# Optimization experiments

Measured on AMD Instinct MI355X. Metric: run time of the kernel, lower is better.

## Reference

```python
import jax, jax.numpy as jnp
import numpy as np

ALPHA = 0.2  # LeakyReLU negative slope
NEG_INF = -1e12


def setup_inputs() -> dict:
    key = jax.random.key(0)
    k1, k2, k3, k4 = jax.random.split(key, 4)
    B, N, F_in, F_out = 8, 4096, 128, 64
    inp = jax.random.normal(k1, (B, N, F_in), dtype=jnp.float32)
    adj = jax.random.randint(k2, (B, N, N), 0, 2, dtype=jnp.int32)
    # xavier-uniform-ish init for W, a
    W = jax.random.normal(k3, (F_in, F_out), dtype=jnp.float32) * (2.0 / (F_in + F_out)) ** 0.5
    a = jax.random.normal(k4, (2 * F_out, 1), dtype=jnp.float32) * (2.0 / (2 * F_out + 1)) ** 0.5
    return {"inp": inp, "adj": adj, "W": W, "a": a}


def reference(inp, adj, W, a):
    # inp: [B,N,F_in], adj: [B,N,N] int, W: [F_in,F_out], a: [2*F_out,1]
    F_out = W.shape[1]
    h = jnp.einsum('bnf,fo->bno', inp, W)          # [B,N,F_out]
    a1 = a[:F_out, 0]                              # [F_out]
    a2 = a[F_out:, 0]                              # [F_out]
    # e[b,i,j] = leakyrelu(h_i . a1 + h_j . a2)  (== concat([h_i,h_j]) @ a)
    s1 = h @ a1                                    # [B,N]
    s2 = h @ a2                                    # [B,N]
    e = s1[:, :, None] + s2[:, None, :]            # [B,N,N]
    e = jnp.where(e > 0, e, ALPHA * e)             # LeakyReLU
    att = jnp.where(adj > 0, e, NEG_INF)
    att = jax.nn.softmax(att, axis=-1)             # [B,N,N]
    # dropout p=0.0 -> identity
    h_prime = jnp.einsum('bij,bjo->bio', att, h)   # [B,N,F_out]
    return jax.nn.elu(h_prime)
```

## Files before the change

### kernel.cpp

```cpp
#include <hip/hip_runtime.h>
#include <hip/hip_bf16.h>
#include <hip/hip_fp16.h>
#include <cstdint>

typedef __attribute__((ext_vector_type(8))) short short8;
typedef __attribute__((ext_vector_type(4))) float floatx4;
typedef __attribute__((ext_vector_type(4))) int   intx4;

#define LEAKY_ALPHA 0.2f

__device__ __forceinline__ unsigned short f2bf_rne(float f) {
    unsigned u = __float_as_uint(f);
    unsigned r = u + 0x7FFFu + ((u >> 16) & 1u);
    return (unsigned short)(r >> 16);
}

__device__ __forceinline__ unsigned pk2bf(float lo, float hi) {
    union { __hip_bfloat162 b; unsigned u; } c;
    c.b = __float22bfloat162_rn(make_float2(lo, hi));
    return c.u;
}

__device__ __forceinline__ float2 h2f2(unsigned w) {
    union { unsigned u; __half2 h; } c; c.u = w;
    return __half22float2(c.h);
}


__global__ __launch_bounds__(256) void k_h(const float* __restrict__ inp,
                                           const float* __restrict__ W,
                                           const float* __restrict__ a,
                                           unsigned short* __restrict__ hT,
                                           float2* __restrict__ e1,
                                           __half2* __restrict__ e2h) {
    __shared__ float hs[64][65];
    const int tid  = threadIdx.x;
    const int wv   = tid >> 6;
    const int lane = tid & 63;
    const int blk  = blockIdx.x;
    const int b     = blk >> 6;
    const int ibase = (blk & 63) * 64;

    const float a1 = a[lane];
    const float a2 = a[64 + lane];

    for (int rr = 0; rr < 16; ++rr) {
        const int rloc = wv * 16 + rr;
        const int row  = ibase + rloc;
        const float* ip = inp + ((size_t)(b * 4096 + row)) * 128;
        float acc = 0.f;
        #pragma unroll
        for (int f = 0; f < 128; f += 4) {
            float4 v = *(const float4*)(ip + f);
            acc += v.x * W[(f + 0) * 64 + lane];
            acc += v.y * W[(f + 1) * 64 + lane];
            acc += v.z * W[(f + 2) * 64 + lane];
            acc += v.w * W[(f + 3) * 64 + lane];
        }
        hs[rloc][lane] = acc;
        float r1 = acc * a1;
        float r2 = acc * a2;
        #pragma unroll
        for (int off = 32; off > 0; off >>= 1) {
            r1 += __shfl_xor(r1, off);
            r2 += __shfl_xor(r2, off);
        }
        if (lane == 0) {
            e1[b * 4096 + row]  = make_float2(__expf(r1), __expf(LEAKY_ALPHA * r1));
            e2h[b * 4096 + row] = __floats2half2_rn(__expf(r2), __expf(LEAKY_ALPHA * r2));
        }
    }
    __syncthreads();

    const int o    = tid & 63;
    const int half = tid >> 6;
    const int tl   = half >> 1;
    const int nco  = (half & 1) * 16;
    unsigned pk[8];
    #pragma unroll
    for (int s = 0; s < 16; s += 2) {
        const int n0 = nco + s, n1 = nco + s + 1;
        const int c0 = 4 * (n0 & 7) + (n0 >> 3);
        const int c1 = 4 * (n1 & 7) + (n1 >> 3);
        unsigned lo = f2bf_rne(hs[tl * 32 + c0][o]);
        unsigned hi = f2bf_rne(hs[tl * 32 + c1][o]);
        pk[s >> 1] = lo | (hi << 16);
    }
    const int tile = (ibase >> 5) + tl;
    unsigned short* dst = hT + (((size_t)b * 128 + tile) * 64 + o) * 32 + nco;
    *(int4*)(dst)     = *(int4*)&pk[0];
    *(int4*)(dst + 8) = *(int4*)&pk[4];
}

__global__ __launch_bounds__(256, 4) void k_fused(const int* __restrict__ adj,
                                                  const unsigned short* __restrict__ hT,
                                                  const float2* __restrict__ e1g,
                                                  const __half2* __restrict__ e2hg,
                                                  float* __restrict__ out) {
    __shared__ unsigned long long mask64[32][16][4];
    __shared__ unsigned e2su[4096];

    const int tid   = threadIdx.x;
    const int b     = blockIdx.x >> 7;
    const int rtile = blockIdx.x & 127;
    const int wv    = tid >> 6;
    const int lane  = tid & 63;

    {
        const unsigned* src = (const unsigned*)(e2hg + b * 4096);
        #pragma unroll
        for (int t = 0; t < 4; ++t) {
            const int c0 = tid * 16 + t * 4;
            const int4 raw = *(const int4*)(src + c0);
            const int base = (c0 & ~31) + ((c0 & 31) >> 2);
            e2su[base +  0] = (unsigned)raw.x;
            e2su[base +  8] = (unsigned)raw.y;
            e2su[base + 16] = (unsigned)raw.z;
            e2su[base + 24] = (unsigned)raw.w;
        }
    }

    {
        const int* abase = adj + ((size_t)(b * 4096 + rtile * 32)) * 4096;
        for (int r = 0; r < 8; ++r) {
            const int lr = wv * 8 + r;
            const int* prow = abase + (size_t)lr * 4096 + lane * 4;
            #pragma unroll 4
            for (int g = 0; g < 16; ++g) {
                const intx4 v = __builtin_nontemporal_load((const intx4*)(prow + g * 256));
                const unsigned long long b0 = __ballot(v.x > 0);
                const unsigned long long b1 = __ballot(v.y > 0);
                const unsigned long long b2 = __ballot(v.z > 0);
                const unsigned long long b3 = __ballot(v.w > 0);
                if (lane == 0) {
                    ulonglong2* d = (ulonglong2*)&mask64[lr][g][0];
                    ulonglong2 t0; t0.x = b0; t0.y = b1;
                    ulonglong2 t1; t1.x = b2; t1.y = b3;
                    d[0] = t0; d[1] = t1;
                }
            }
        }
    }

    const int jhalf = wv >> 1;
    const int m     = lane & 15;
    const int kh    = lane >> 4;
    const int rl    = (wv & 1) * 16 + m;
    const int rbase = rtile * 32 + (wv & 1) * 16;
    const int row   = rbase + m;

    const float2 E1 = e1g[b * 4096 + row];
    const float E1p = E1.x, E1n = E1.y;
    const int jb0 = jhalf * 2048 + kh * 8;

    const unsigned short* hbase =
        hT + (((size_t)b * 128 + jhalf * 64) * 64 + m) * 32 + kh * 8;
    const unsigned short* hrow0 = hbase;
    const unsigned short* hrow1 = hbase + 512;
    const unsigned short* hrow2 = hbase + 1024;
    const unsigned short* hrow3 = hbase + 1536;

    floatx4 acc0 = (floatx4){0.f,0.f,0.f,0.f};
    floatx4 acc1 = (floatx4){0.f,0.f,0.f,0.f};
    floatx4 acc2 = (floatx4){0.f,0.f,0.f,0.f};
    floatx4 acc3 = (floatx4){0.f,0.f,0.f,0.f};
    float lsum = 0.f;

    short8 rb0_0, rb1_0, rb2_0, rb3_0, rb0_1, rb1_1, rb2_1, rb3_1;
    rb0_0 = *(const short8*)(hrow0);         rb1_0 = *(const short8*)(hrow1);
    rb2_0 = *(const short8*)(hrow2);         rb3_0 = *(const short8*)(hrow3);
    rb0_1 = *(const short8*)(hrow0 + 2048);  rb1_1 = *(const short8*)(hrow1 + 2048);
    rb2_1 = *(const short8*)(hrow2 + 2048);  rb3_1 = *(const short8*)(hrow3 + 2048);

    __syncthreads();

#define GAT_COL(WRD, T)                                                        \
    {                                                                          \
        const float2 ef = h2f2((unsigned)(WRD));                               \
        const float P  = E1p * ef.x;                                           \
        const float Nn = E1n * ef.y;                                           \
        float p = (P > 1.0f) ? P : Nn;                                         \
        p = ((mb >> (T)) & 1u) ? p : 0.0f;                                     \
        psum += p;                                                             \
        pv[T] = p;                                                             \
    }

#define GAT_STEP(SL, STEPIDX)                                                  \
    do {                                                                       \
        const short8 cb0 = rb0_##SL, cb1 = rb1_##SL;                           \
        const short8 cb2 = rb2_##SL, cb3 = rb3_##SL;                           \
        const int pstep = ((STEPIDX) + 2) & 63;         \
        const int poff = pstep * 2048;                         \
        rb0_##SL = *(const short8*)(hrow0 + poff);                             \
        rb1_##SL = *(const short8*)(hrow1 + poff);                             \
        rb2_##SL = *(const short8*)(hrow2 + poff);                             \
        rb3_##SL = *(const short8*)(hrow3 + poff);                             \
        const int soff = jb0 + (STEPIDX) * 32;                                 \
        const int4 eA = *(const int4*)&e2su[soff];                             \
        const int4 eB = *(const int4*)&e2su[soff + 4];                         \
        const unsigned mb = (unsigned)(Mcur >> (8 * ((STEPIDX) & 7))) & 0xffu; \
        float pv[8];                                                           \
        float psum = 0.f;                                                      \
        GAT_COL(eA.x, 0) GAT_COL(eA.y, 1) GAT_COL(eA.z, 2) GAT_COL(eA.w, 3)    \
        GAT_COL(eB.x, 4) GAT_COL(eB.y, 5) GAT_COL(eB.z, 6) GAT_COL(eB.w, 7)    \
        lsum += psum;                                                          \
        int4 ai;                                                               \
        ai.x = pk2bf(pv[0], pv[1]); ai.y = pk2bf(pv[2], pv[3]);                \
        ai.z = pk2bf(pv[4], pv[5]); ai.w = pk2bf(pv[6], pv[7]);                \
        union { int4 i; short8 s; } cc; cc.i = ai;                             \
        const short8 af = cc.s;                                                \
        acc0 = __builtin_amdgcn_mfma_f32_16x16x32_bf16(af, cb0, acc0, 0,0,0);  \
        acc1 = __builtin_amdgcn_mfma_f32_16x16x32_bf16(af, cb1, acc1, 0,0,0);  \
        acc2 = __builtin_amdgcn_mfma_f32_16x16x32_bf16(af, cb2, acc2, 0,0,0);  \
        acc3 = __builtin_amdgcn_mfma_f32_16x16x32_bf16(af, cb3, acc3, 0,0,0);  \
    } while (0)

    #pragma unroll 1
    for (int p = 0; p < 8; ++p) {
        const unsigned long long Mcur =
            *(const unsigned long long*)&mask64[rl][jhalf * 8 + p][kh];
        #pragma unroll
        for (int q = 0; q < 4; ++q) {
            GAT_STEP(0, p * 8 + 2 * q);
            GAT_STEP(1, p * 8 + 2 * q + 1);
        }
    }
#undef GAT_STEP
#undef GAT_COL

    lsum += __shfl_xor(lsum, 16);
    lsum += __shfl_xor(lsum, 32);

    floatx4 accs[4] = {acc0, acc1, acc2, acc3};

    float* accb = (float*)&mask64[0][0][0];
    float* lb   = accb + 2 * 64 * 17;

    __syncthreads();
    if (wv >= 2) {
        #pragma unroll
        for (int f = 0; f < 4; ++f)
            #pragma unroll
            for (int r = 0; r < 4; ++r)
                accb[(wv - 2) * 64 * 17 + lane * 17 + f * 4 + r] = accs[f][r];
        lb[(wv - 2) * 64 + lane] = lsum;
    }
    __syncthreads();
    if (wv < 2) {
        const float ltot = lsum + lb[wv * 64 + lane];
        #pragma unroll
        for (int f = 0; f < 4; ++f) {
            #pragma unroll
            for (int r = 0; r < 4; ++r) {
                float v = accs[f][r] + accb[wv * 64 * 17 + lane * 17 + f * 4 + r];
                const int drow = (lane >> 4) * 4 + r;
                const float lr = __shfl(ltot, drow);
                const float hp = v / lr;
                const float o  = (hp > 0.f) ? hp : (__expf(hp) - 1.f);
                out[((size_t)(b * 4096 + rbase + drow)) * 64 + f * 16 + (lane & 15)] = o;
            }
        }
    }
}

extern "C" void kernel_launch(void* const* d_in, const int* in_sizes, int n_in,
                              void* d_out, int out_size, void* d_ws, size_t ws_size,
                              hipStream_t stream) {
    const float* inp = (const float*)d_in[0];
    const int*   adj = (const int*)d_in[1];
    const float* W   = (const float*)d_in[2];
    const float* a   = (const float*)d_in[3];
    float* out = (float*)d_out;

    unsigned short* hT = (unsigned short*)d_ws;
    float2*  e1  = (float2*)((char*)d_ws + (size_t)4 * 1024 * 1024);
    __half2* e2h = (__half2*)((char*)d_ws + (size_t)4 * 1024 * 1024 + 262144);

    k_h<<<512, 256, 0, stream>>>(inp, W, a, hT, e1, e2h);
    k_fused<<<1024, 256, 0, stream>>>(adj, hT, e1, e2h, out);
}
```

Before: 790.7 us.

## Overlap adjacency mask packing with attention MFMA loop via software pipelining

Moves the adjacency-to-bitmask packing out of the prologue and interleaves it with the main gather/MFMA loop. Each iteration prefetches the next 256-column group of adj rows while computing on the current group. Wave pairs now split columns by interleaved 32-column parity instead of contiguous halves, so each mask group is consumed right after it is built. This aims to hide the large adj HBM read latency behind compute, at the cost of more live registers (eight intx4 loads in flight) and a __syncthreads per group.

After: 830.0 us. 5.0% more time.

```diff
diff --git a/kernel.cpp b/kernel.cpp
--- a/kernel.cpp
+++ b/kernel.cpp
@@ -106,6 +106,62 @@
     const int wv    = tid >> 6;
     const int lane  = tid & 63;
 
+    const int par  = wv >> 1;
+    const int m    = lane & 15;
+    const int kh   = lane >> 4;
+    const int khs  = kh << 3;
+    const int sh8  = par << 3;
+    const int rl   = (wv & 1) * 16 + m;
+    const int rbase = rtile * 32 + (wv & 1) * 16;
+    const int row   = rbase + m;
+
+    const int* pA = adj + ((size_t)(b * 4096 + rtile * 32 + wv * 8)) * 4096 + lane * 4;
+
+    intx4 av0, av1, av2, av3, av4, av5, av6, av7;
+
+#define PACK_ISSUE_LO(GOFF)                                                    \
+    do {                                                                       \
+        const int* pg = pA + (GOFF);                                           \
+        av0 = __builtin_nontemporal_load((const intx4*)(pg + 0 * 4096));       \
+        av1 = __builtin_nontemporal_load((const intx4*)(pg + 1 * 4096));       \
+        av2 = __builtin_nontemporal_load((const intx4*)(pg + 2 * 4096));       \
+        av3 = __builtin_nontemporal_load((const intx4*)(pg + 3 * 4096));       \
+    } while (0)
+
+#define PACK_ISSUE_HI(GOFF)                                                    \
+    do {                                                                       \
+        const int* pg = pA + (GOFF);                                           \
+        av4 = __builtin_nontemporal_load((const intx4*)(pg + 4 * 4096));       \
+        av5 = __builtin_nontemporal_load((const intx4*)(pg + 5 * 4096));       \
+        av6 = __builtin_nontemporal_load((const intx4*)(pg + 6 * 4096));       \
+        av7 = __builtin_nontemporal_load((const intx4*)(pg + 7 * 4096));       \
+    } while (0)
+
+#define PB_ROW(R, G, AV)                                                       \
+    {                                                                          \
+        const unsigned long long b0 = __ballot(AV.x > 0);                      \
+        const unsigned long long b1 = __ballot(AV.y > 0);                      \
+        const unsigned long long b2 = __ballot(AV.z > 0);                      \
+        const unsigned long long b3 = __ballot(AV.w > 0);                      \
+        if (lane == 0) {                                                       \
+            ulonglong2* d = (ulonglong2*)&mask64[wv * 8 + (R)][(G)][0];        \
+            ulonglong2 t0; t0.x = b0; t0.y = b1;                               \
+            ulonglong2 t1; t1.x = b2; t1.y = b3;                               \
+            d[0] = t0; d[1] = t1;                                              \
+        }                                                                      \
+    }
+
+#define PACK_BALLOT_LO(G)                                                      \
+    do { PB_ROW(0, G, av0) PB_ROW(1, G, av1)                                   \
+         PB_ROW(2, G, av2) PB_ROW(3, G, av3) } while (0)
+
+#define PACK_BALLOT_HI(G)                                                      \
+    do { PB_ROW(4, G, av4) PB_ROW(5, G, av5)                                   \
+         PB_ROW(6, G, av6) PB_ROW(7, G, av7) } while (0)
+
+    PACK_ISSUE_LO(0);
+    PACK_ISSUE_HI(0);
+
     {
         const unsigned* src = (const unsigned*)(e2hg + b * 4096);
         #pragma unroll
@@ -120,41 +176,11 @@
         }
     }
 
-    {
-        const int* abase = adj + ((size_t)(b * 4096 + rtile * 32)) * 4096;
-        for (int r = 0; r < 8; ++r) {
-            const int lr = wv * 8 + r;
-            const int* prow = abase + (size_t)lr * 4096 + lane * 4;
-            #pragma unroll 4
-            for (int g = 0; g < 16; ++g) {
-                const intx4 v = __builtin_nontemporal_load((const intx4*)(prow + g * 256));
-                const unsigned long long b0 = __ballot(v.x > 0);
-                const unsigned long long b1 = __ballot(v.y > 0);
-                const unsigned long long b2 = __ballot(v.z > 0);
-                const unsigned long long b3 = __ballot(v.w > 0);
-                if (lane == 0) {
-                    ulonglong2* d = (ulonglong2*)&mask64[lr][g][0];
-                    ulonglong2 t0; t0.x = b0; t0.y = b1;
-                    ulonglong2 t1; t1.x = b2; t1.y = b3;
-                    d[0] = t0; d[1] = t1;
-                }
-            }
-        }
-    }
-
-    const int jhalf = wv >> 1;
-    const int m     = lane & 15;
-    const int kh    = lane >> 4;
-    const int rl    = (wv & 1) * 16 + m;
-    const int rbase = rtile * 32 + (wv & 1) * 16;
-    const int row   = rbase + m;
-
     const float2 E1 = e1g[b * 4096 + row];
     const float E1p = E1.x, E1n = E1.y;
-    const int jb0 = jhalf * 2048 + kh * 8;
 
     const unsigned short* hbase =
-        hT + (((size_t)b * 128 + jhalf * 64) * 64 + m) * 32 + kh * 8;
+        hT + (((size_t)b * 128) * 64 + m) * 32 + khs;
     const unsigned short* hrow0 = hbase;
     const unsigned short* hrow1 = hbase + 512;
     const unsigned short* hrow2 = hbase + 1024;
@@ -167,11 +193,16 @@
     float lsum = 0.f;
 
     short8 rb0_0, rb1_0, rb2_0, rb3_0, rb0_1, rb1_1, rb2_1, rb3_1;
-    rb0_0 = *(const short8*)(hrow0);         rb1_0 = *(const short8*)(hrow1);
-    rb2_0 = *(const short8*)(hrow2);         rb3_0 = *(const short8*)(hrow3);
-    rb0_1 = *(const short8*)(hrow0 + 2048);  rb1_1 = *(const short8*)(hrow1 + 2048);
-    rb2_1 = *(const short8*)(hrow2 + 2048);  rb3_1 = *(const short8*)(hrow3 + 2048);
-
+    {
+        const int p0 = par * 2048, p1 = (2 + par) * 2048;
+        rb0_0 = *(const short8*)(hrow0 + p0); rb1_0 = *(const short8*)(hrow1 + p0);
+        rb2_0 = *(const short8*)(hrow2 + p0); rb3_0 = *(const short8*)(hrow3 + p0);
+        rb0_1 = *(const short8*)(hrow0 + p1); rb1_1 = *(const short8*)(hrow1 + p1);
+        rb2_1 = *(const short8*)(hrow2 + p1); rb3_1 = *(const short8*)(hrow3 + p1);
+    }
+
+    PACK_BALLOT_LO(0);
+    PACK_BALLOT_HI(0);
     __syncthreads();
 
 #define GAT_COL(WRD, T)                                                        \
@@ -185,20 +216,20 @@
         pv[T] = p;                                                             \
     }
 
-#define GAT_STEP(SL, STEPIDX)                                                  \
+#define GAT_STEP(SL, Q)                                                        \
     do {                                                                       \
         const short8 cb0 = rb0_##SL, cb1 = rb1_##SL;                           \
         const short8 cb2 = rb2_##SL, cb3 = rb3_##SL;                           \
-        const int pstep = ((STEPIDX) + 2) & 63;         \
-        const int poff = pstep * 2048;                         \
+        const int jc   = jb + 2 * (Q);                                         \
+        const int poff = ((jc + 4) & 127) * 2048;       \
         rb0_##SL = *(const short8*)(hrow0 + poff);                             \
         rb1_##SL = *(const short8*)(hrow1 + poff);                             \
         rb2_##SL = *(const short8*)(hrow2 + poff);                             \
         rb3_##SL = *(const short8*)(hrow3 + poff);                             \
-        const int soff = jb0 + (STEPIDX) * 32;                                 \
+        const int soff = jc * 32 + khs;                                        \
         const int4 eA = *(const int4*)&e2su[soff];                             \
         const int4 eB = *(const int4*)&e2su[soff + 4];                         \
-        const unsigned mb = (unsigned)(Mcur >> (8 * ((STEPIDX) & 7))) & 0xffu; \
+        const unsigned mb = (unsigned)(Mcur >> (((Q) << 4) + sh8)) & 0xffu;    \
         float pv[8];                                                           \
         float psum = 0.f;                                                      \
         GAT_COL(eA.x, 0) GAT_COL(eA.y, 1) GAT_COL(eA.z, 2) GAT_COL(eA.w, 3)    \
@@ -216,13 +247,22 @@
     } while (0)
 
     #pragma unroll 1
-    for (int p = 0; p < 8; ++p) {
+    for (int g = 0; g < 16; ++g) {
+        if (g < 15) PACK_ISSUE_LO((g + 1) << 8);
+        const int jb = g * 8 + par;
         const unsigned long long Mcur =
-            *(const unsigned long long*)&mask64[rl][jhalf * 8 + p][kh];
-        #pragma unroll
-        for (int q = 0; q < 4; ++q) {
-            GAT_STEP(0, p * 8 + 2 * q);
-            GAT_STEP(1, p * 8 + 2 * q + 1);
+            *(const unsigned long long*)&mask64[rl][g][kh];
+        GAT_STEP(0, 0);
+        GAT_STEP(1, 1);
+        if (g < 15) {
+            PACK_ISSUE_HI((g + 1) << 8);
+            PACK_BALLOT_LO(g + 1);
+        }
+        GAT_STEP(0, 2);
+        GAT_STEP(1, 3);
+        if (g < 15) {
+            PACK_BALLOT_HI(g + 1);
+            __syncthreads();
         }
     }
 #undef GAT_STEP
```

## Warp-specialize: producer waves stream adjacency mask while consumer waves compute

Applied to the files above, without the earlier changes.

Splits the block into producer waves that convert adjacency chunks into bitmasks and consumer waves that run the attention/MFMA accumulation over the full column range. Chunks are pipelined with block barriers so the adjacency load overlaps compute, and the cross-wave partial-sum reduction is removed. In exchange only half the waves do MFMA work, and the producers are limited to two waves issuing the large adj stream.

New measurement: 772.6 us (median of 2 runs). 1.02x faster.

```diff
diff --git a/kernel.cpp b/kernel.cpp
--- a/kernel.cpp
+++ b/kernel.cpp
@@ -105,6 +105,9 @@
     const int rtile = blockIdx.x & 127;
     const int wv    = tid >> 6;
     const int lane  = tid & 63;
+    const int m     = lane & 15;
+    const int kh    = lane >> 4;
+    const int khs   = kh << 3;
 
     {
         const unsigned* src = (const unsigned*)(e2hg + b * 4096);
@@ -120,41 +123,15 @@
         }
     }
 
-    {
-        const int* abase = adj + ((size_t)(b * 4096 + rtile * 32)) * 4096;
-        for (int r = 0; r < 8; ++r) {
-            const int lr = wv * 8 + r;
-            const int* prow = abase + (size_t)lr * 4096 + lane * 4;
-            #pragma unroll 4
-            for (int g = 0; g < 16; ++g) {
-                const intx4 v = __builtin_nontemporal_load((const intx4*)(prow + g * 256));
-                const unsigned long long b0 = __ballot(v.x > 0);
-                const unsigned long long b1 = __ballot(v.y > 0);
-                const unsigned long long b2 = __ballot(v.z > 0);
-                const unsigned long long b3 = __ballot(v.w > 0);
-                if (lane == 0) {
-                    ulonglong2* d = (ulonglong2*)&mask64[lr][g][0];
-                    ulonglong2 t0; t0.x = b0; t0.y = b1;
-                    ulonglong2 t1; t1.x = b2; t1.y = b3;
-                    d[0] = t0; d[1] = t1;
-                }
-            }
-        }
-    }
-
-    const int jhalf = wv >> 1;
-    const int m     = lane & 15;
-    const int kh    = lane >> 4;
+    const int prow0 = (wv >= 2) ? ((wv - 2) * 16) : 0;
+    const int* pA = adj + ((size_t)(b * 4096 + rtile * 32 + prow0)) * 4096 + lane * 4;
+
     const int rl    = (wv & 1) * 16 + m;
     const int rbase = rtile * 32 + (wv & 1) * 16;
-    const int row   = rbase + m;
-
-    const float2 E1 = e1g[b * 4096 + row];
+    const float2 E1 = e1g[b * 4096 + rbase + m];
     const float E1p = E1.x, E1n = E1.y;
-    const int jb0 = jhalf * 2048 + kh * 8;
-
-    const unsigned short* hbase =
-        hT + (((size_t)b * 128 + jhalf * 64) * 64 + m) * 32 + kh * 8;
+
+    const unsigned short* hbase = hT + (((size_t)b * 128) * 64 + m) * 32 + khs;
     const unsigned short* hrow0 = hbase;
     const unsigned short* hrow1 = hbase + 512;
     const unsigned short* hrow2 = hbase + 1024;
@@ -172,6 +149,47 @@
     rb0_1 = *(const short8*)(hrow0 + 2048);  rb1_1 = *(const short8*)(hrow1 + 2048);
     rb2_1 = *(const short8*)(hrow2 + 2048);  rb3_1 = *(const short8*)(hrow3 + 2048);
 
+#define PB1(LR, G, AV)                                                         \
+    {                                                                          \
+        const unsigned long long b0 = __ballot(AV.x > 0);                      \
+        const unsigned long long b1 = __ballot(AV.y > 0);                      \
+        const unsigned long long b2 = __ballot(AV.z > 0);                      \
+        const unsigned long long b3 = __ballot(AV.w > 0);                      \
+        if (lane == 0) {                                                       \
+            ulonglong2* d = (ulonglong2*)&mask64[LR][G][0];                    \
+            ulonglong2 t0; t0.x = b0; t0.y = b1;                               \
+            ulonglong2 t1; t1.x = b2; t1.y = b3;                               \
+            d[0] = t0; d[1] = t1;                                              \
+        }                                                                      \
+    }
+
+#define PRODUCE_SG(SG)                                                         \
+    do {                                                                       \
+        const int* ps = pA + (SG) * 1024;                                      \
+        _Pragma("unroll 2")                                                    \
+        for (int r = 0; r < 16; r += 2) {                                      \
+            const int* p0 = ps + (size_t)r * 4096;                             \
+            const int* p1 = p0 + 4096;                                         \
+            const intx4 a0 = __builtin_nontemporal_load((const intx4*)(p0));       \
+            const intx4 a1 = __builtin_nontemporal_load((const intx4*)(p0 + 256)); \
+            const intx4 a2 = __builtin_nontemporal_load((const intx4*)(p0 + 512)); \
+            const intx4 a3 = __builtin_nontemporal_load((const intx4*)(p0 + 768)); \
+            const intx4 a4 = __builtin_nontemporal_load((const intx4*)(p1));       \
+            const intx4 a5 = __builtin_nontemporal_load((const intx4*)(p1 + 256)); \
+            const intx4 a6 = __builtin_nontemporal_load((const intx4*)(p1 + 512)); \
+            const intx4 a7 = __builtin_nontemporal_load((const intx4*)(p1 + 768)); \
+            PB1(prow0 + r,     (SG) * 4 + 0, a0)                               \
+            PB1(prow0 + r,     (SG) * 4 + 1, a1)                               \
+            PB1(prow0 + r,     (SG) * 4 + 2, a2)                               \
+            PB1(prow0 + r,     (SG) * 4 + 3, a3)                               \
+            PB1(prow0 + r + 1, (SG) * 4 + 0, a4)                               \
+            PB1(prow0 + r + 1, (SG) * 4 + 1, a5)                               \
+            PB1(prow0 + r + 1, (SG) * 4 + 2, a6)                               \
+            PB1(prow0 + r + 1, (SG) * 4 + 3, a7)                               \
+        }                                                                      \
+    } while (0)
+
+    if (wv >= 2) PRODUCE_SG(0);
     __syncthreads();
 
 #define GAT_COL(WRD, T)                                                        \
@@ -185,20 +203,19 @@
         pv[T] = p;                                                             \
     }
 
-#define GAT_STEP(SL, STEPIDX)                                                  \
+#define GAT_STEP(SL, JC, TT)                                                   \
     do {                                                                       \
         const short8 cb0 = rb0_##SL, cb1 = rb1_##SL;                           \
         const short8 cb2 = rb2_##SL, cb3 = rb3_##SL;                           \
-        const int pstep = ((STEPIDX) + 2) & 63;         \
-        const int poff = pstep * 2048;                         \
+        const int poff = (((JC) + 2) & 127) * 2048;     \
         rb0_##SL = *(const short8*)(hrow0 + poff);                             \
         rb1_##SL = *(const short8*)(hrow1 + poff);                             \
         rb2_##SL = *(const short8*)(hrow2 + poff);                             \
         rb3_##SL = *(const short8*)(hrow3 + poff);                             \
-        const int soff = jb0 + (STEPIDX) * 32;                                 \
+        const int soff = (JC) * 32 + khs;                                      \
         const int4 eA = *(const int4*)&e2su[soff];                             \
         const int4 eB = *(const int4*)&e2su[soff + 4];                         \
-        const unsigned mb = (unsigned)(Mcur >> (8 * ((STEPIDX) & 7))) & 0xffu; \
+        const unsigned mb = (unsigned)(Mcur >> (8 * (TT))) & 0xffu;            \
         float pv[8];                                                           \
         float psum = 0.f;                                                      \
         GAT_COL(eA.x, 0) GAT_COL(eA.y, 1) GAT_COL(eA.z, 2) GAT_COL(eA.w, 3)    \
@@ -216,48 +233,44 @@
     } while (0)
 
     #pragma unroll 1
-    for (int p = 0; p < 8; ++p) {
-        const unsigned long long Mcur =
-            *(const unsigned long long*)&mask64[rl][jhalf * 8 + p][kh];
-        #pragma unroll
-        for (int q = 0; q < 4; ++q) {
-            GAT_STEP(0, p * 8 + 2 * q);
-            GAT_STEP(1, p * 8 + 2 * q + 1);
-        }
+    for (int sg = 0; sg < 4; ++sg) {
+        if (wv >= 2) {
+            if (sg < 3) PRODUCE_SG(sg + 1);
+        } else {
+            #pragma unroll
+            for (int g4 = 0; g4 < 4; ++g4) {
+                const int g = sg * 4 + g4;
+                const unsigned long long Mcur =
+                    *(const unsigned long long*)&mask64[rl][g][kh];
+                const int j0 = g * 8;
+                GAT_STEP(0, j0 + 0, 0); GAT_STEP(1, j0 + 1, 1);
+                GAT_STEP(0, j0 + 2, 2); GAT_STEP(1, j0 + 3, 3);
+                GAT_STEP(0, j0 + 4, 4); GAT_STEP(1, j0 + 5, 5);
+                GAT_STEP(0, j0 + 6, 6); GAT_STEP(1, j0 + 7, 7);
+            }
+        }
+        if (sg < 3) __syncthreads();
     }
 #undef GAT_STEP
 #undef GAT_COL
-
-    lsum += __shfl_xor(lsum, 16);
-    lsum += __shfl_xor(lsum, 32);
-
-    floatx4 accs[4] = {acc0, acc1, acc2, acc3};
-
-    float* accb = (float*)&mask64[0][0][0];
-    float* lb   = accb + 2 * 64 * 17;
-
-    __syncthreads();
-    if (wv >= 2) {
-        #pragma unroll
-        for (int f = 0; f < 4; ++f)
-            #pragma unroll
-            for (int r = 0; r < 4; ++r)
-                accb[(wv - 2) * 64 * 17 + lane * 17 + f * 4 + r] = accs[f][r];
-        lb[(wv - 2) * 64 + lane] = lsum;
-    }
-    __syncthreads();
+#undef PRODUCE_SG
+#undef PB1
+
     if (wv < 2) {
-        const float ltot = lsum + lb[wv * 64 + lane];
+        lsum += __shfl_xor(lsum, 16);
+        lsum += __shfl_xor(lsum, 32);
+        const float ltot = lsum;
+        floatx4 accs[4] = {acc0, acc1, acc2, acc3};
         #pragma unroll
         for (int f = 0; f < 4; ++f) {
             #pragma unroll
             for (int r = 0; r < 4; ++r) {
-                float v = accs[f][r] + accb[wv * 64 * 17 + lane * 17 + f * 4 + r];
-                const int drow = (lane >> 4) * 4 + r;
+                const int drow = kh * 4 + r;
                 const float lr = __shfl(ltot, drow);
+                const float v  = accs[f][r];
                 const float hp = v / lr;
                 const float o  = (hp > 0.f) ? hp : (__expf(hp) - 1.f);
-                out[((size_t)(b * 4096 + rbase + drow)) * 64 + f * 16 + (lane & 15)] = o;
+                out[((size_t)(b * 4096 + rbase + drow)) * 64 + f * 16 + m] = o;
             }
         }
     }
```
